# Kernel optimization log

Hardware: AMD Instinct MI355X
Metric: run time of the kernel (lower is better)

The kernel has to match this reference:

```python
import jax, jax.numpy as jnp
import numpy as np


def setup_inputs() -> dict:
    key = jax.random.key(0)
    ks = jax.random.split(key, 8)
    B, C, W, H = 4, 256, 64, 64
    dqk = C // 8
    s_in = 1.0 / np.sqrt(C)
    return {
        "x": jax.random.normal(ks[0], (B, C, W, H), dtype=jnp.float32),
        "Wq": jax.random.normal(ks[1], (dqk, C), dtype=jnp.float32) * s_in,
        "bq": jnp.zeros((dqk,), dtype=jnp.float32),
        "Wk": jax.random.normal(ks[2], (dqk, C), dtype=jnp.float32) * s_in,
        "bk": jnp.zeros((dqk,), dtype=jnp.float32),
        "Wv": jax.random.normal(ks[3], (C, C), dtype=jnp.float32) * s_in,
        "bv": jnp.zeros((C,), dtype=jnp.float32),
        "gamma": jnp.zeros((1,), dtype=jnp.float32),
    }


def reference(x, Wq, bq, Wk, bk, Wv, bv, gamma):
    B, C, W, H = x.shape
    N = W * H
    xf = x.reshape(B, C, N)  # flatten spatial: B x C x N
    # 1x1 convs == per-pixel linear projections over channels
    q = jnp.einsum("bcn,dc->bnd", xf, Wq) + bq            # B x N x dqk
    k = jnp.einsum("bcn,dc->bdn", xf, Wk) + bk[None, :, None]  # B x dqk x N
    v = jnp.einsum("bcn,dc->bdn", xf, Wv) + bv[None, :, None]  # B x C x N
    # unscaled attention, softmax over keys (last dim)
    attn = jax.nn.softmax(jnp.einsum("bnd,bdm->bnm", q, k), axis=-1)  # B x N x N
    # out[b,c,i] = sum_j v[b,c,j] * attn[b,i,j]  (bmm with attn^T)
    out = jnp.einsum("bcj,bij->bci", v, attn).reshape(B, C, W, H)
    return gamma[0] * out + x
```

## Files before the change

kernel.cpp:

```cpp
#include <hip/hip_runtime.h>

#define BB 4
#define CC 256
#define NN 4096

typedef __attribute__((ext_vector_type(8))) short bh8;
typedef __attribute__((ext_vector_type(4))) float f32x4;

#define WPK_OFF  0
#define BALL_OFF 163840
#define QBF_OFF  165888
#define KBF_OFF  (165888 + 1048576)
#define VBF_OFF  (165888 + 2097152)

typedef const __attribute__((address_space(1))) void* gas_t;
typedef __attribute__((address_space(3))) void* las_t;
__device__ inline void gld16(const void* g, void* l) {
    __builtin_amdgcn_global_load_lds((gas_t)g, (las_t)l, 16, 0, 0);
}

__device__ inline int pack2bf(float a, float b) {
    unsigned ua = __builtin_bit_cast(unsigned, a) + 0x8000u;
    unsigned ub = __builtin_bit_cast(unsigned, b) + 0x8000u;
    return (int)__builtin_amdgcn_perm(ub, ua, 0x07060302u);
}
__device__ inline short f2bf1(float a) {
    return (short)((__builtin_bit_cast(unsigned, a) + 0x8000u) >> 16);
}

__global__ __launch_bounds__(256) void prep_w(const float* __restrict__ Wq,
        const float* __restrict__ bq, const float* __restrict__ Wk,
        const float* __restrict__ bk, const float* __restrict__ Wv,
        const float* __restrict__ bv, short* __restrict__ Wpk,
        float* __restrict__ ball) {
    int tid = blockIdx.x * 256 + threadIdx.x;
    if (tid < 10240) {
        int lane = tid & 63;
        int fc = tid >> 6;
        int mt = fc >> 3, ck = fc & 7;
        int m = mt * 16 + (lane & 15);
        int c0 = ck * 32 + (lane >> 4) * 8;
        const float* wrow;
        if (m < 32)      wrow = Wq + m * 256;
        else if (m < 64) wrow = Wk + (m - 32) * 256;
        else             wrow = Wv + (m - 64) * 256;
        int d[4];
        #pragma unroll
        for (int p = 0; p < 4; ++p)
            d[p] = pack2bf(wrow[c0 + 2 * p], wrow[c0 + 2 * p + 1]);
        *(int4*)(Wpk + tid * 8) = make_int4(d[0], d[1], d[2], d[3]);
    }
    if (tid < 320) {
        float b2 = tid < 32 ? bq[tid] : (tid < 64 ? bk[tid - 32] : bv[tid - 64]);
        ball[tid] = b2;
    }
}

__global__ __launch_bounds__(256) void proj(const float* __restrict__ x,
        const short* __restrict__ Wpk, const float* __restrict__ ball,
        short* __restrict__ qbf, short* __restrict__ kbf,
        short* __restrict__ vbf) {
    int t = threadIdx.x;
    int w = t >> 6, lane = t & 63, quad = lane >> 4, c15 = lane & 15;
    int gw = blockIdx.x * 4 + w;
    int tile = gw >> 1, mh = gw & 1;
    int b = tile >> 8, n0 = (tile & 255) * 16;
    const float* xb = x + (size_t)b * CC * NN;

    bh8 af[8];
    #pragma unroll
    for (int ck = 0; ck < 8; ++ck) {
        float v[8];
        #pragma unroll
        for (int e = 0; e < 8; ++e)
            v[e] = xb[(size_t)(ck * 32 + quad * 8 + e) * NN + n0 + c15];
        int d[4];
        #pragma unroll
        for (int p = 0; p < 4; ++p) d[p] = pack2bf(v[2 * p], v[2 * p + 1]);
        af[ck] = __builtin_bit_cast(bh8, make_int4(d[0], d[1], d[2], d[3]));
    }

    #pragma unroll
    for (int mpi = 0; mpi < 5; ++mpi) {
        int mp = mh * 5 + mpi;
        int mtA = mp * 2, mtB = mp * 2 + 1;
        float blA = ball[mtA * 16 + c15], blB = ball[mtB * 16 + c15];
        f32x4 accA = {blA, blA, blA, blA}, accB = {blB, blB, blB, blB};
        #pragma unroll
        for (int ck = 0; ck < 8; ++ck) {
            bh8 wfA = *(const bh8*)(Wpk + ((mtA * 8 + ck) * 64 + lane) * 8);
            bh8 wfB = *(const bh8*)(Wpk + ((mtB * 8 + ck) * 64 + lane) * 8);
            accA = __builtin_amdgcn_mfma_f32_16x16x32_bf16(af[ck], wfA, accA, 0, 0, 0);
            accB = __builtin_amdgcn_mfma_f32_16x16x32_bf16(af[ck], wfB, accB, 0, 0, 0);
        }
        #pragma unroll
        for (int half = 0; half < 2; ++half) {
            int mt = mp * 2 + half;
            f32x4 acc = half ? accB : accA;
            if (mt < 4) {
                short* dst = (mt < 2) ? qbf : kbf;
                int m = (mt & 1) * 16 + c15;
                #pragma unroll
                for (int r = 0; r < 4; ++r)
                    dst[(size_t)(b * NN + n0 + quad * 4 + r) * 32 + m] = f2bf1(acc[r]);
            } else {
                int c = mt * 16 + c15 - 64;
                int2 pk;
                pk.x = pack2bf(acc[0], acc[1]);
                pk.y = pack2bf(acc[2], acc[3]);
                *(int2*)(vbf + (size_t)b * CC * NN + (size_t)c * NN + n0 + quad * 4) = pk;
            }
        }
    }
}

__global__ __launch_bounds__(512, 2) void flash_attn(
        const short* __restrict__ qbf, const short* __restrict__ kbf,
        const short* __restrict__ vbf, const float* __restrict__ x,
        const float* __restrict__ gamma, float* __restrict__ out) {
    __shared__ char lds[148480];

    int bid = blockIdx.x;
    int b = bid & 3, i0 = (bid >> 2) * 64;
    int t = threadIdx.x;
    int w = t >> 6, lane = t & 63, quad = lane >> 4, c15 = lane & 15;
    int mg = w & 3, nh = w >> 2, jsub = w & 3;

    const short* qb = qbf + (size_t)b * NN * 32;
    const short* kb = kbf + (size_t)b * NN * 32;
    const short* vb = vbf + (size_t)b * CC * NN;

    bh8 qf0 = *(const bh8*)(qb + (size_t)(i0 + nh * 32 + c15) * 32 + quad * 8);
    bh8 qf1 = *(const bh8*)(qb + (size_t)(i0 + nh * 32 + 16 + c15) * 32 + quad * 8);

    int vrow = w * 32 + (lane >> 3);
    int glog = (lane & 7) ^ ((lane >> 3) & 7);
    const short* vsg = vb + (size_t)vrow * NN + glog * 8;
    char* vdst = lds + w * 4096;

    const short* kptr = kb + (size_t)(jsub * 16 + c15) * 32 + quad * 8;

    char* Pt = lds + 131072;
    float* lred = (float*)(lds + 147456);

    f32x4 acc[4][2];
    #pragma unroll
    for (int ms = 0; ms < 4; ++ms) {
        acc[ms][0] = (f32x4){0.f, 0.f, 0.f, 0.f};
        acc[ms][1] = (f32x4){0.f, 0.f, 0.f, 0.f};
    }
    float lsum0 = 0.f, lsum1 = 0.f;
    const f32x4 initc = {-12.f, -12.f, -12.f, -12.f};

    bh8 kf = *(const bh8*)kptr;
    #pragma unroll
    for (int s = 0; s < 3; ++s) {
        #pragma unroll
        for (int r = 0; r < 4; ++r)
            gld16(vsg + s * 64 + r * 8 * NN, lds + s * 32768 + w * 4096 + r * 1024);
    }

    int vcur = 0, vnx = 3;
    for (int jt = 0; jt < 64; ++jt) {
        int cur = jt & 1;
        bh8 kfn = *(const bh8*)(kptr + (size_t)((jt + 1) & 63) * 2048);

        f32x4 sa0 = __builtin_amdgcn_mfma_f32_16x16x32_bf16(kf, qf0, initc, 0, 0, 0);
        f32x4 sa1 = __builtin_amdgcn_mfma_f32_16x16x32_bf16(kf, qf1, initc, 0, 0, 0);
        float p0[4], p1[4];
        #pragma unroll
        for (int r = 0; r < 4; ++r) {
            p0[r] = __expf(sa0[r]); lsum0 += p0[r];
            p1[r] = __expf(sa1[r]); lsum1 += p1[r];
        }
        char* Ptc = Pt + cur * 8192;
        int g = jsub * 2 + (quad >> 1);
        int pb0 = (nh * 32 + c15) * 128 + ((g ^ (c15 & 7)) * 16) + (quad & 1) * 8;
        *(int2*)(Ptc + pb0) = make_int2(pack2bf(p0[0], p0[1]), pack2bf(p0[2], p0[3]));
        *(int2*)(Ptc + pb0 + 2048) = make_int2(pack2bf(p1[0], p1[1]), pack2bf(p1[2], p1[3]));

        asm volatile("s_waitcnt vmcnt(9) lgkmcnt(0)" ::: "memory");
        __builtin_amdgcn_sched_barrier(0);
        __builtin_amdgcn_s_barrier();
        __builtin_amdgcn_sched_barrier(0);

        {
            const short* vs = vsg + (size_t)((jt + 3) & 63) * 64;
            char* vd = lds + vnx * 32768 + w * 4096;
            #pragma unroll
            for (int r = 0; r < 4; ++r) gld16(vs + r * 8 * NN, vd + r * 1024);
        }

        const char* Vb = lds + vcur * 32768;
        #pragma unroll
        for (int kk = 0; kk < 2; ++kk) {
            int gs = ((kk * 4 + quad) ^ (c15 & 7)) * 16;
            bh8 pfa = *(const bh8*)(Ptc + (nh * 32 + c15) * 128 + gs);
            bh8 pfb = *(const bh8*)(Ptc + (nh * 32 + 16 + c15) * 128 + gs);
            #pragma unroll
            for (int ms = 0; ms < 4; ++ms) {
                int c = mg * 64 + ms * 16 + c15;
                bh8 vf = *(const bh8*)(Vb + c * 128 + gs);
                acc[ms][0] = __builtin_amdgcn_mfma_f32_16x16x32_bf16(vf, pfa, acc[ms][0], 0, 0, 0);
                acc[ms][1] = __builtin_amdgcn_mfma_f32_16x16x32_bf16(vf, pfb, acc[ms][1], 0, 0, 0);
            }
        }
        kf = kfn;
        vcur = (vcur + 1) & 3;
        vnx  = (vnx + 1) & 3;
    }

    lsum0 += __shfl_xor(lsum0, 16); lsum0 += __shfl_xor(lsum0, 32);
    lsum1 += __shfl_xor(lsum1, 16); lsum1 += __shfl_xor(lsum1, 32);
    __syncthreads();
    if (lane < 16) {
        lred[w * 32 + lane] = lsum0;
        lred[w * 32 + 16 + lane] = lsum1;
    }
    __syncthreads();
    float l0 = lred[(nh * 4 + 0) * 32 + c15] + lred[(nh * 4 + 1) * 32 + c15]
             + lred[(nh * 4 + 2) * 32 + c15] + lred[(nh * 4 + 3) * 32 + c15];
    float l1 = lred[(nh * 4 + 0) * 32 + 16 + c15] + lred[(nh * 4 + 1) * 32 + 16 + c15]
             + lred[(nh * 4 + 2) * 32 + 16 + c15] + lred[(nh * 4 + 3) * 32 + 16 + c15];
    float linv0 = 1.0f / l0, linv1 = 1.0f / l1;

    float gm = gamma[0];
    const float* xb2 = x + (size_t)b * CC * NN;
    float* ob = out + (size_t)b * CC * NN;
    int ia = i0 + nh * 32 + c15, ib2 = ia + 16;
    #pragma unroll
    for (int ms = 0; ms < 4; ++ms) {
        #pragma unroll
        for (int r = 0; r < 4; ++r) {
            int c = mg * 64 + ms * 16 + quad * 4 + r;
            ob[(size_t)c * NN + ia]  = gm * acc[ms][0][r] * linv0 + xb2[(size_t)c * NN + ia];
            ob[(size_t)c * NN + ib2] = gm * acc[ms][1][r] * linv1 + xb2[(size_t)c * NN + ib2];
        }
    }
}

extern "C" void kernel_launch(void* const* d_in, const int* in_sizes, int n_in,
                              void* d_out, int out_size, void* d_ws, size_t ws_size,
                              hipStream_t stream) {
    const float* x     = (const float*)d_in[0];
    const float* Wq    = (const float*)d_in[1];
    const float* bq    = (const float*)d_in[2];
    const float* Wk    = (const float*)d_in[3];
    const float* bk    = (const float*)d_in[4];
    const float* Wv    = (const float*)d_in[5];
    const float* bv    = (const float*)d_in[6];
    const float* gamma = (const float*)d_in[7];
    float* out = (float*)d_out;
    char*  ws  = (char*)d_ws;
    short* Wpk  = (short*)(ws + WPK_OFF);
    float* ball = (float*)(ws + BALL_OFF);
    short* qbf  = (short*)(ws + QBF_OFF);
    short* kbf  = (short*)(ws + KBF_OFF);
    short* vbf  = (short*)(ws + VBF_OFF);

    prep_w<<<40, 256, 0, stream>>>(Wq, bq, Wk, bk, Wv, bv, Wpk, ball);
    proj<<<512, 256, 0, stream>>>(x, Wpk, ball, qbf, kbf, vbf);
    flash_attn<<<256, 512, 0, stream>>>(qbf, kbf, vbf, x, gamma, out);
}
```

Baseline: 154.6 us.

## Stage K tiles through LDS with async global_load_lds double buffering

K fragments were loaded per wave straight from global memory into registers. They are now loaded asynchronously into a double-buffered, swizzled LDS region using global_load_lds, issued alongside the V prefetch, and read from LDS each iteration. The vmcnt wait thresholds change, and the LDS footprint grows so lred can reuse the start of LDS. This aims to take global-load latency off the QK critical path. In exchange it adds an extra prologue barrier and more LDS pressure, which could lower occupancy below 2 blocks per CU.

```diff
diff --git a/kernel.cpp b/kernel.cpp
--- a/kernel.cpp
+++ b/kernel.cpp
@@ -118,7 +118,7 @@
         const short* __restrict__ qbf, const short* __restrict__ kbf,
         const short* __restrict__ vbf, const float* __restrict__ x,
         const float* __restrict__ gamma, float* __restrict__ out) {
-    __shared__ char lds[148480];
+    __shared__ char lds[155648];
 
     int bid = blockIdx.x;
     int b = bid & 3, i0 = (bid >> 2) * 64;
@@ -136,12 +136,17 @@
     int vrow = w * 32 + (lane >> 3);
     int glog = (lane & 7) ^ ((lane >> 3) & 7);
     const short* vsg = vb + (size_t)vrow * NN + glog * 8;
-    char* vdst = lds + w * 4096;
-
-    const short* kptr = kb + (size_t)(jsub * 16 + c15) * 32 + quad * 8;
-
-    char* Pt = lds + 131072;
-    float* lred = (float*)(lds + 147456);
+
+    int wk = w & 3;
+    int krow = lane >> 2;
+    int kslot = (lane & 3) ^ (krow & 3);
+    const short* ksg = kb + (size_t)(wk * 16 + krow) * 32 + kslot * 8;
+
+    int kr = jsub * 16 + c15;
+    int krd = kr * 64 + ((quad ^ (kr & 3)) << 4);
+
+    char* Pt = lds + 139264;
+    float* lred = (float*)lds;
 
     f32x4 acc[4][2];
     #pragma unroll
@@ -152,19 +157,23 @@
     float lsum0 = 0.f, lsum1 = 0.f;
     const f32x4 initc = {-12.f, -12.f, -12.f, -12.f};
 
-    bh8 kf = *(const bh8*)kptr;
+    gld16(ksg, lds + 131072 + wk * 1024);
+    gld16(ksg + 2048, lds + 131072 + 4096 + wk * 1024);
     #pragma unroll
     for (int s = 0; s < 3; ++s) {
         #pragma unroll
         for (int r = 0; r < 4; ++r)
             gld16(vsg + s * 64 + r * 8 * NN, lds + s * 32768 + w * 4096 + r * 1024);
     }
-
-    int vcur = 0, vnx = 3;
+    asm volatile("s_waitcnt vmcnt(0)" ::: "memory");
+    __builtin_amdgcn_sched_barrier(0);
+    __builtin_amdgcn_s_barrier();
+    __builtin_amdgcn_sched_barrier(0);
+    asm volatile("" : "+v"(qf0), "+v"(qf1));
+
     for (int jt = 0; jt < 64; ++jt) {
         int cur = jt & 1;
-        bh8 kfn = *(const bh8*)(kptr + (size_t)((jt + 1) & 63) * 2048);
-
+        bh8 kf = *(const bh8*)(lds + 131072 + cur * 4096 + krd);
         f32x4 sa0 = __builtin_amdgcn_mfma_f32_16x16x32_bf16(kf, qf0, initc, 0, 0, 0);
         f32x4 sa1 = __builtin_amdgcn_mfma_f32_16x16x32_bf16(kf, qf1, initc, 0, 0, 0);
         float p0[4], p1[4];
@@ -179,19 +188,22 @@
         *(int2*)(Ptc + pb0) = make_int2(pack2bf(p0[0], p0[1]), pack2bf(p0[2], p0[3]));
         *(int2*)(Ptc + pb0 + 2048) = make_int2(pack2bf(p1[0], p1[1]), pack2bf(p1[2], p1[3]));
 
-        asm volatile("s_waitcnt vmcnt(9) lgkmcnt(0)" ::: "memory");
+        asm volatile("s_waitcnt vmcnt(4) lgkmcnt(0)" ::: "memory");
         __builtin_amdgcn_sched_barrier(0);
         __builtin_amdgcn_s_barrier();
         __builtin_amdgcn_sched_barrier(0);
 
+        gld16(ksg + (size_t)((jt + 2) & 63) * 2048,
+              lds + 131072 + cur * 4096 + wk * 1024);
         {
             const short* vs = vsg + (size_t)((jt + 3) & 63) * 64;
-            char* vd = lds + vnx * 32768 + w * 4096;
+            char* vd = lds + (size_t)((jt + 3) & 3) * 32768 + w * 4096;
             #pragma unroll
             for (int r = 0; r < 4; ++r) gld16(vs + r * 8 * NN, vd + r * 1024);
         }
-
-        const char* Vb = lds + vcur * 32768;
+        __builtin_amdgcn_sched_barrier(0);
+
+        const char* Vb = lds + (size_t)(jt & 3) * 32768;
         #pragma unroll
         for (int kk = 0; kk < 2; ++kk) {
             int gs = ((kk * 4 + quad) ^ (c15 & 7)) * 16;
@@ -205,9 +217,6 @@
                 acc[ms][1] = __builtin_amdgcn_mfma_f32_16x16x32_bf16(vf, pfb, acc[ms][1], 0, 0, 0);
             }
         }
-        kf = kfn;
-        vcur = (vcur + 1) & 3;
-        vnx  = (vnx + 1) & 3;
     }
 
     lsum0 += __shfl_xor(lsum0, 16); lsum0 += __shfl_xor(lsum0, 32);
```

Result: faster. 146.1 us (-5.6%).
